# Kernel tuning notes

Measured on AMD Instinct MI355X. Metric: run time of the kernel, lower is better.

The kernel has to match this reference:

```python
import jax, jax.numpy as jnp
import numpy as np

DIM = 640
HEADS = 8
HEAD_DIM = 80
CROSS = 768
FF_INNER = 4 * DIM  # 2560
EPS = 1e-5
SCALE = HEAD_DIM ** -0.5


def _ln(x, w, b):
    m = jnp.mean(x, axis=-1, keepdims=True)
    v = jnp.var(x, axis=-1, keepdims=True)
    return (x - m) * jax.lax.rsqrt(v + EPS) * w + b


def _split_heads(x):  # [B,S,D] -> [B,H,S,dh]
    B, S, D = x.shape
    return x.reshape(B, S, HEADS, D // HEADS).transpose(0, 2, 1, 3)


def _merge_heads(x):  # [B,H,S,dh] -> [B,S,D]
    B, H, S, dh = x.shape
    return x.transpose(0, 2, 1, 3).reshape(B, S, H * dh)


def _mha(q, k, v):
    # q:[B,S,D] k,v:[B,Skv,D]
    qh, kh, vh = _split_heads(q), _split_heads(k), _split_heads(v)
    scores = jnp.einsum('bhqd,bhkd->bhqk', qh, kh) * SCALE
    probs = jax.nn.softmax(scores, axis=-1)
    out = jnp.einsum('bhqk,bhkd->bhqd', probs, vh)
    return _merge_heads(out)


def _forward(hidden_states, encoder_hidden_states, video_length, p):
    BF, S, D = hidden_states.shape
    f = video_length
    b = BF // f

    # ---- attn1: sparse causal self-attention ----
    x = _ln(hidden_states, p['ln1_w'], p['ln1_b'])
    q = x @ p['q1']
    k = x @ p['k1']
    v = x @ p['v1']
    former = jnp.concatenate([jnp.zeros((1,), jnp.int32), jnp.arange(f - 1, dtype=jnp.int32)])
    def gather_kv(t):  # [BF,S,D] -> [BF,2S,D]
        t = t.reshape(b, f, S, D)
        first = jnp.broadcast_to(t[:, 0:1], (b, f, S, D))
        prev = t[:, former]
        return jnp.concatenate([first, prev], axis=2).reshape(BF, 2 * S, D)
    k = gather_kv(k)
    v = gather_kv(v)
    attn1 = _mha(q, k, v) @ p['o1_w'] + p['o1_b']
    hidden_states = attn1 + hidden_states

    # ---- attn2: cross attention to text ----
    x = _ln(hidden_states, p['ln2_w'], p['ln2_b'])
    q = x @ p['q2']
    k = encoder_hidden_states @ p['k2']
    v = encoder_hidden_states @ p['v2']
    attn2 = _mha(q, k, v) @ p['o2_w'] + p['o2_b']
    hidden_states = attn2 + hidden_states

    # ---- feed-forward (geglu) ----
    x = _ln(hidden_states, p['ln3_w'], p['ln3_b'])
    proj = x @ p['ff_w1'] + p['ff_b1']
    h, gate = jnp.split(proj, 2, axis=-1)
    ff = (h * jax.nn.gelu(gate)) @ p['ff_w2'] + p['ff_b2']
    return ff + hidden_states


def setup_inputs() -> dict:
    key = jax.random.key(0)
    ks = jax.random.split(key, 20)
    s = lambda i, shape, scale=0.02: jax.random.normal(ks[i], shape, jnp.float32) * scale
    inp = {
        'hidden_states': jax.random.normal(ks[0], (8, 1024, DIM), jnp.float32),
        'encoder_hidden_states': jax.random.normal(ks[1], (8, 77, CROSS), jnp.float32),
        'video_length': 8,
        'ln1_w': jnp.ones((DIM,)), 'ln1_b': jnp.zeros((DIM,)),
        'q1': s(2, (DIM, DIM)), 'k1': s(3, (DIM, DIM)), 'v1': s(4, (DIM, DIM)),
        'o1_w': s(5, (DIM, DIM)), 'o1_b': jnp.zeros((DIM,)),
        'ln2_w': jnp.ones((DIM,)), 'ln2_b': jnp.zeros((DIM,)),
        'q2': s(6, (DIM, DIM)), 'k2': s(7, (CROSS, DIM)), 'v2': s(8, (CROSS, DIM)),
        'o2_w': s(9, (DIM, DIM)), 'o2_b': jnp.zeros((DIM,)),
        'ln3_w': jnp.ones((DIM,)), 'ln3_b': jnp.zeros((DIM,)),
        'ff_w1': s(10, (DIM, 2 * FF_INNER)), 'ff_b1': jnp.zeros((2 * FF_INNER,)),
        'ff_w2': s(11, (FF_INNER, DIM)), 'ff_b2': jnp.zeros((DIM,)),
    }
    return inp


def reference(hidden_states, encoder_hidden_states, video_length,
              ln1_w, ln1_b, q1, k1, v1, o1_w, o1_b,
              ln2_w, ln2_b, q2, k2, v2, o2_w, o2_b,
              ln3_w, ln3_b, ff_w1, ff_b1, ff_w2, ff_b2):
    p = dict(ln1_w=ln1_w, ln1_b=ln1_b, q1=q1, k1=k1, v1=v1, o1_w=o1_w, o1_b=o1_b,
             ln2_w=ln2_w, ln2_b=ln2_b, q2=q2, k2=k2, v2=v2, o2_w=o2_w, o2_b=o2_b,
             ln3_w=ln3_w, ln3_b=ln3_b, ff_w1=ff_w1, ff_b1=ff_b1, ff_w2=ff_w2, ff_b2=ff_b2)
    return _forward(hidden_states, encoder_hidden_states, video_length, p)
```

## Files before the change

### kernel.cpp

```cpp
#include <hip/hip_runtime.h>
#include <stdint.h>

#define TOK   8192
#define DIM   640
#define HEADS 8
#define HD    80
#define SEQ   1024
#define CROSS 768
#define ETOK  616
#define FFI   2560
#define SCALE 0.11180339887498949f

typedef unsigned short u16;
typedef unsigned int   u32;

using bf8   = __attribute__((ext_vector_type(8))) short;
using f32x4 = __attribute__((ext_vector_type(4))) float;

struct __align__(16) U4 { u32 x, y, z, w; };
struct __align__(8)  U2 { u32 x, y; };

__device__ __forceinline__ float bf2f(u16 u){
  union { u32 i; float f; } v; v.i = ((u32)u) << 16; return v.f;
}
__device__ __forceinline__ u16 f2bf(float f){
  union { float f; u32 i; } v; v.f = f;
  u32 r = v.i + 0x7fffu + ((v.i >> 16) & 1u);
  return (u16)(r >> 16);
}
__device__ __forceinline__ u32 cvtpk_bf16(float lo, float hi){
  u32 r; asm("v_cvt_pk_bf16_f32 %0, %1, %2" : "=v"(r) : "v"(lo), "v"(hi)); return r;
}
__device__ __forceinline__ float gelu_t(float x){
  float y = 0.7978845608028654f * (x + 0.044715f * x * x * x);
  float e = __expf(2.f * y);
  return 0.5f * x * (2.f - 2.f / (e + 1.f));
}

__device__ __forceinline__ void gl2lds16(const u16* g, u16* l){
  __builtin_amdgcn_global_load_lds(
      (const __attribute__((address_space(1))) void*)g,
      (__attribute__((address_space(3))) void*)l, 16, 0, 0);
}

__global__ void zero_k(u16* p){ p[threadIdx.x] = 0; }

struct CvtJob  { const float* s; u16* d; int n; };
struct CvtJobs { CvtJob j[11]; };
__global__ __launch_bounds__(256) void cvt_all(CvtJobs jobs)
{
  const CvtJob jb = jobs.j[blockIdx.y];
  for (long i = (long)blockIdx.x*256 + threadIdx.x; i < jb.n; i += (long)gridDim.x*256)
    jb.d[i] = f2bf(jb.s[i]);
}

struct TJob  { const float* s; u16* d; int R, C, srcLd, dstLd; };
struct TJobs { TJob j[10]; };
__global__ __launch_bounds__(256) void transpose_tiled(TJobs jobs)
{
  const TJob jb = jobs.j[blockIdx.y];
  const int tilesC = jb.C >> 6;
  const int nt = (jb.R >> 6) * tilesC;
  if ((int)blockIdx.x >= nt) return;
  const int tr = (blockIdx.x / tilesC) << 6, tc = (blockIdx.x % tilesC) << 6;
  __shared__ u16 t[64][65];
  const int tid = threadIdx.x;
  const int rr = tid >> 3, c8 = (tid & 7) * 8;
  #pragma unroll
  for (int p = 0; p < 2; ++p){
    const int r = rr + p*32;
    const float* s = &jb.s[(long)(tr + r)*jb.srcLd + tc + c8];
    #pragma unroll
    for (int j = 0; j < 8; ++j) t[r][c8 + j] = f2bf(s[j]);
  }
  __syncthreads();
  #pragma unroll
  for (int p = 0; p < 2; ++p){
    const int c = rr + p*32;
    u16 tmp[8];
    #pragma unroll
    for (int j = 0; j < 8; ++j) tmp[j] = t[c8 + j][c];
    *(U4*)&jb.d[(long)(tc + c)*jb.dstLd + tr + c8] = *(U4*)tmp;
  }
}

__global__ __launch_bounds__(256) void transpose_geglu(
    const float* __restrict__ src, u16* __restrict__ dst)
{
  __shared__ u16 t[64][65];
  const int ir0 = blockIdx.x << 6, k0 = blockIdx.y << 6;
  const int hc0 = ir0 >> 1;
  const int tid = threadIdx.x;
  const int rr = tid >> 3, c8 = (tid & 7) * 8;
  #pragma unroll
  for (int p = 0; p < 2; ++p){
    const int k = rr + p*32;
    const int scol = (c8 < 32) ? (hc0 + c8) : (FFI + hc0 + (c8 - 32));
    const float* s = &src[(long)(k0 + k)*(2*FFI) + scol];
    #pragma unroll
    for (int j = 0; j < 8; ++j){
      const int lc = c8 + j;
      const int grp = (lc < 32) ? 0 : 1;
      const int lg  = lc - grp*32;
      const int irl = (lg >> 4)*32 + grp*16 + (lg & 15);
      t[k][irl] = f2bf(s[j]);
    }
  }
  __syncthreads();
  #pragma unroll
  for (int p = 0; p < 2; ++p){
    const int c = rr + p*32;
    u16 tmp[8];
    #pragma unroll
    for (int j = 0; j < 8; ++j) tmp[j] = t[c8 + j][c];
    *(U4*)&dst[(long)(ir0 + c)*DIM + k0 + c8] = *(U4*)tmp;
  }
}

__global__ __launch_bounds__(256) void transpose_tile(
    const u16* __restrict__ src, u16* __restrict__ dst,
    int srcLd, int dstLd)
{
  __shared__ u16 t[64][65];
  const int tr = blockIdx.y << 6, tc = blockIdx.x << 6;
  const int tid = threadIdx.x;
  const int rr = tid >> 3, c8 = (tid & 7) * 8;
  #pragma unroll
  for (int p = 0; p < 2; ++p){
    const int r = rr + p*32;
    U4 v = *(const U4*)&src[(long)(tr + r)*srcLd + tc + c8];
    const u16* pv = (const u16*)&v;
    #pragma unroll
    for (int j = 0; j < 8; ++j) t[r][c8 + j] = pv[j];
  }
  __syncthreads();
  #pragma unroll
  for (int p = 0; p < 2; ++p){
    const int c = rr + p*32;
    u16 tmp[8];
    #pragma unroll
    for (int j = 0; j < 8; ++j) tmp[j] = t[c8 + j][c];
    *(U4*)&dst[(long)(tc + c)*dstLd + tr + c8] = *(U4*)tmp;
  }
}

__global__ __launch_bounds__(256) void transpose_v2(
    const u16* __restrict__ src, u16* __restrict__ dst)
{
  int idx = blockIdx.x*256 + threadIdx.x;
  if (idx >= DIM*640) return;
  int d = idx / 640, c = idx - d*640;
  int g = c / 80, j = c - g*80;
  u16 v = 0;
  if (j < 77) v = src[(long)(g*77 + j)*(2*DIM) + DIM + d];
  dst[(long)d*640 + c] = v;
}

__global__ __launch_bounds__(256) void ln_k(
    const void* __restrict__ src, const u16* __restrict__ w,
    const u16* __restrict__ b, u16* __restrict__ dst, int srcf32)
{
  const int wave = threadIdx.x >> 6, lane = threadIdx.x & 63;
  const long row = (long)blockIdx.x*4 + wave;
  float x[10];
  if (srcf32){
    const float* s = (const float*)src + row*DIM;
    #pragma unroll
    for (int j = 0; j < 5; ++j){
      float2 v = *(const float2*)&s[lane*2 + j*128];
      x[j*2] = v.x; x[j*2+1] = v.y;
    }
  } else {
    const u16* s = (const u16*)src + row*DIM;
    #pragma unroll
    for (int j = 0; j < 5; ++j){
      u32 v = *(const u32*)&s[lane*2 + j*128];
      x[j*2]   = bf2f((u16)(v & 0xffffu));
      x[j*2+1] = bf2f((u16)(v >> 16));
    }
  }
  float sum = 0.f;
  #pragma unroll
  for (int i = 0; i < 10; ++i) sum += x[i];
  #pragma unroll
  for (int d = 1; d < 64; d <<= 1) sum += __shfl_xor(sum, d, 64);
  const float mean = sum * (1.f/DIM);
  float vq = 0.f;
  #pragma unroll
  for (int i = 0; i < 10; ++i){ float dd = x[i] - mean; vq += dd*dd; }
  #pragma unroll
  for (int d = 1; d < 64; d <<= 1) vq += __shfl_xor(vq, d, 64);
  const float rs = rsqrtf(vq * (1.f/DIM) + 1e-5f);
  u16* q = dst + row*DIM;
  #pragma unroll
  for (int j = 0; j < 5; ++j){
    const int off = lane*2 + j*128;
    u32 wv = *(const u32*)&w[off];
    u32 bv = *(const u32*)&b[off];
    float o0 = (x[j*2]   - mean)*rs*bf2f((u16)(wv & 0xffffu)) + bf2f((u16)(bv & 0xffffu));
    float o1 = (x[j*2+1] - mean)*rs*bf2f((u16)(wv >> 16))     + bf2f((u16)(bv >> 16));
    *(u32*)&q[off] = (u32)f2bf(o0) | ((u32)f2bf(o1) << 16);
  }
}

template<int BN>
__global__ __launch_bounds__(256) void gemm_bt(
    const u16* __restrict__ A, const u16* __restrict__ BT, void* __restrict__ C,
    int M, int N, int K, int lda, int ldb, int ldc,
    const u16* __restrict__ bias, const void* __restrict__ res, int ldr,
    int resf32, int outf32)
{
  constexpr int NT  = BN/32;
  constexpr int BCH = BN/16;
  constexpr int BPW = BCH/4;
  constexpr int LPW = 2 + BPW;
  __shared__ __align__(16) u16 sA[3][8*512];
  __shared__ __align__(16) u16 sB[3][BCH*512];
  const int tid  = threadIdx.x;
  const int wave = tid >> 6, lane = tid & 63;
  const int quad = lane >> 4, l16 = lane & 15;
  const int m0 = blockIdx.y * 128, n0 = blockIdx.x * BN;
  const int wm = (wave >> 1) * 64, wn = (wave & 1) * (BN/2);
  const int srow = lane & 15;
  const int scol = (lane >> 4) * 8;

  long aoff[2];
  #pragma unroll
  for (int i = 0; i < 2; ++i){
    int r = m0 + (wave*2 + i)*16 + srow;
    r = r < M ? r : M - 1;
    aoff[i] = (long)r*lda + scol;
  }
  long boff[BPW];
  #pragma unroll
  for (int i = 0; i < BPW; ++i){
    int r = n0 + (wave*BPW + i)*16 + srow;
    boff[i] = (long)r*ldb + scol;
  }

  auto stage = [&](int ks, int buf){
    const int kk = ks*32;
    #pragma unroll
    for (int i = 0; i < 2; ++i)   gl2lds16(&A[aoff[i] + kk],  &sA[buf][(wave*2 + i)*512]);
    #pragma unroll
    for (int i = 0; i < BPW; ++i) gl2lds16(&BT[boff[i] + kk], &sB[buf][(wave*BPW + i)*512]);
  };

  const int NS = K >> 5;
  f32x4 acc[4][NT] = {};
  stage(0, 0);
  if (NS > 1) stage(1, 1);

  int cur = 0;
  for (int ks = 0; ks < NS; ++ks){
    if (ks < NS - 1) asm volatile("s_waitcnt vmcnt(%0)" :: "n"(LPW) : "memory");
    else             asm volatile("s_waitcnt vmcnt(0)" ::: "memory");
    __builtin_amdgcn_sched_barrier(0);
    __builtin_amdgcn_s_barrier();
    __builtin_amdgcn_sched_barrier(0);
    if (ks + 2 < NS){
      int nbuf = cur + 2; if (nbuf >= 3) nbuf -= 3;
      stage(ks + 2, nbuf);
    }
    bf8 a[4], b[NT];
    #pragma unroll
    for (int mt = 0; mt < 4; ++mt)  a[mt] = *(const bf8*)&sA[cur][((wm>>4) + mt)*512 + lane*8];
    #pragma unroll
    for (int nt = 0; nt < NT; ++nt) b[nt] = *(const bf8*)&sB[cur][((wn>>4) + nt)*512 + lane*8];
    #pragma unroll
    for (int mt = 0; mt < 4; ++mt)
      #pragma unroll
      for (int nt = 0; nt < NT; ++nt)
        acc[mt][nt] = __builtin_amdgcn_mfma_f32_16x16x32_bf16(a[mt], b[nt], acc[mt][nt], 0, 0, 0);
    cur = (cur == 2) ? 0 : cur + 1;
  }
  #pragma unroll
  for (int mt = 0; mt < 4; ++mt){
    const int rl = wm + mt*16 + quad*4;
    #pragma unroll
    for (int nt = 0; nt < NT; ++nt){
      const int col = n0 + wn + nt*16 + l16;
      float bv = bias ? bf2f(bias[col]) : 0.f;
      #pragma unroll
      for (int r = 0; r < 4; ++r){
        int row = m0 + rl + r;
        if (row < M){
          float v = acc[mt][nt][r] + bv;
          if (res) v += resf32 ? ((const float*)res)[(long)row*ldr + col]
                               : bf2f(((const u16*)res)[(long)row*ldr + col]);
          if (outf32) ((float*)C)[(long)row*ldc + col] = v;
          else        ((u16*)C) [(long)row*ldc + col] = f2bf(v);
        }
      }
    }
  }
}

__global__ __launch_bounds__(256) void gemm_geglu(
    const u16* __restrict__ A, const u16* __restrict__ W, u16* __restrict__ C,
    const u16* __restrict__ bias)
{
  __shared__ __align__(16) u16 sA[2][8*512];
  __shared__ __align__(16) u16 sB[2][8*512];
  const int tid  = threadIdx.x;
  const int wave = tid >> 6, lane = tid & 63;
  const int quad = lane >> 4, l16 = lane & 15;
  const int m0 = blockIdx.y * 128, n0 = blockIdx.x * 128;
  const int wm = (wave >> 1) * 64, wn = (wave & 1) * 64;
  const int srow = lane & 15;
  const int scol = (lane >> 4) * 8;

  long aoff[2], boff[2];
  #pragma unroll
  for (int i = 0; i < 2; ++i){
    aoff[i] = (long)(m0 + (wave*2 + i)*16 + srow)*DIM + scol;
    boff[i] = (long)(n0 + (wave*2 + i)*16 + srow)*DIM + scol;
  }

  f32x4 acc[4][4] = {};
  #pragma unroll
  for (int i = 0; i < 2; ++i){
    gl2lds16(&A[aoff[i]], &sA[0][(wave*2 + i)*512]);
    gl2lds16(&W[boff[i]], &sB[0][(wave*2 + i)*512]);
  }
  __syncthreads();

  int cur = 0;
  for (int k0 = 0; ; ){
    const int kn = k0 + 32;
    if (kn < DIM){
      #pragma unroll
      for (int i = 0; i < 2; ++i){
        gl2lds16(&A[aoff[i] + kn], &sA[cur^1][(wave*2 + i)*512]);
        gl2lds16(&W[boff[i] + kn], &sB[cur^1][(wave*2 + i)*512]);
      }
    }
    bf8 a[4], b[4];
    #pragma unroll
    for (int mt = 0; mt < 4; ++mt) a[mt] = *(const bf8*)&sA[cur][((wm>>4) + mt)*512 + lane*8];
    #pragma unroll
    for (int nt = 0; nt < 4; ++nt) b[nt] = *(const bf8*)&sB[cur][((wn>>4) + nt)*512 + lane*8];
    #pragma unroll
    for (int mt = 0; mt < 4; ++mt)
      #pragma unroll
      for (int nt = 0; nt < 4; ++nt)
        acc[mt][nt] = __builtin_amdgcn_mfma_f32_16x16x32_bf16(a[mt], b[nt], acc[mt][nt], 0, 0, 0);
    k0 = kn;
    if (k0 >= DIM) break;
    __syncthreads();
    cur ^= 1;
  }
  #pragma unroll
  for (int mt = 0; mt < 4; ++mt){
    const int rl = wm + mt*16 + quad*4;
    #pragma unroll
    for (int p = 0; p < 2; ++p){
      const int col = ((n0 + wn) >> 1) + p*16 + l16;
      const float bh = bf2f(bias[col]);
      const float bg = bf2f(bias[FFI + col]);
      #pragma unroll
      for (int r = 0; r < 4; ++r){
        int row = m0 + rl + r;
        float h = acc[mt][2*p][r]   + bh;
        float g = acc[mt][2*p+1][r] + bg;
        C[(long)row*FFI + col] = f2bf(h * gelu_t(g));
      }
    }
  }
}

template<int MODE>
__global__ __launch_bounds__(256) void attn_k(
    const u16* __restrict__ qbuf, const u16* __restrict__ kbuf,
    const u16* __restrict__ vT, u16* __restrict__ out,
    const u16* __restrict__ zblk)
{
  constexpr int QLD  = MODE ? DIM      : 3*DIM;
  constexpr int KLD  = MODE ? 2*DIM    : 3*DIM;
  constexpr int KCOL = MODE ? 0        : DIM;
  constexpr int VLD  = MODE ? DIM      : TOK;
  constexpr int NK   = MODE ? 77       : 2*SEQ;
  constexpr int NCH  = MODE ? 3        : 64;
  constexpr float C1   = SCALE * 1.4426950408889634f;
  constexpr float THRR = 8.0f / C1;

  const int qt = blockIdx.x, h = blockIdx.y, g = blockIdx.z;
  const int tid = threadIdx.x, wave = tid >> 6, lane = tid & 63;
  const int quad = lane >> 4, l16 = lane & 15;

  __shared__ __align__(16) u16 Kb[2][6*512];
  __shared__ __align__(16) u16 Vb[2][5*512];
  __shared__ __align__(16) u16 Ps[4][16*40];

  const int qrow0 = g*SEQ + qt*64;
  bf8 qf[3];
  {
    const long qbase = (long)(qrow0 + wave*16 + l16)*QLD + h*HD;
    #pragma unroll
    for (int ks = 0; ks < 3; ++ks){
      const int d = ks*32 + quad*8;
      const u16* src = (d < HD) ? &qbuf[qbase + d] : zblk;
      qf[ks] = *(const bf8*)src;
    }
  }

  const int former = (g == 0) ? 0 : (g - 1);

  const bool kc1v = (wave < 2);
  const int  vc0  = (wave + 2) & 3;
  const bool vc1v = (wave == 2);

  long ko[2] = {0,0}, koB[2] = {0,0}, vo[2] = {0,0}, voB[2] = {0,0};
  bool koob[2];
  #pragma unroll
  for (int j = 0; j < 2; ++j){
    const int ci = wave + 4*j;
    const int ck = ci/3, ks = ci - ck*3;
    const int d = ks*32 + quad*8;
    koob[j] = (d >= HD);
    if (MODE == 0){
      const int dcl = koob[j] ? 0 : d;
      const int row = ck*16 + l16;
      ko[j]  = (long)row*KLD + KCOL + h*HD + dcl;
      koB[j] = ko[j] + (long)former*SEQ*KLD;
    }
  }
  if (MODE == 0){
    vo[0]  = (long)(h*HD + vc0*16 + l16)*VLD + quad*8;
    vo[1]  = (long)(h*HD + 64    + l16)*VLD + quad*8;
    voB[0] = vo[0] + (long)former*SEQ;
    voB[1] = vo[1] + (long)former*SEQ;
  }

  auto stageM0 = [&](int buf){
    gl2lds16(koob[0] ? zblk : &kbuf[ko[0]], &Kb[buf][(wave)*512]);
    if (kc1v) gl2lds16(koob[1] ? zblk : &kbuf[ko[1]], &Kb[buf][(wave+4)*512]);
    gl2lds16(&vT[vo[0]], &Vb[buf][vc0*512]);
    if (vc1v) gl2lds16(&vT[vo[1]], &Vb[buf][4*512]);
    ko[0] += 32L*KLD; ko[1] += 32L*KLD;
    vo[0] += 32; vo[1] += 32;
  };
  auto stageM1 = [&](int c, int buf){
    #pragma unroll
    for (int ci = 0; ci < 6; ++ci){
      if ((ci & 3) == wave){
        const int ck = ci / 3, ks = ci % 3;
        const int d  = ks*32 + quad*8;
        const int rl = ck*16 + l16;
        int j = c*32 + rl; j = j < NK ? j : NK-1;
        const u16* src = (d < HD) ? &kbuf[((long)g*77 + j)*KLD + KCOL + h*HD + d] : zblk;
        gl2lds16(src, &Kb[buf][ci*512]);
      }
    }
    #pragma unroll
    for (int vi = 0; vi < 5; ++vi){
      if (((vi + 2) & 3) == wave){
        const int dd = vi*16 + l16;
        int key = c*32 + quad*8;
        const u16* src = (key < 80) ? &vT[(long)(h*HD + dd)*VLD + g*80 + key] : zblk;
        gl2lds16(src, &Vb[buf][vi*512]);
      }
    }
  };

  f32x4 o[5] = {};
  float mrun = -1e30f, lrun = 0.f, nmc = 0.f;

  if (MODE == 0) stageM0(0); else stageM1(0, 0);
  __syncthreads();
  int cur = 0;

  for (int c = 0; c < NCH; ++c){
    if (c + 1 < NCH){
      if (MODE == 0){
        if (c + 1 == 32){
          ko[0] = koB[0]; ko[1] = koB[1];
          vo[0] = voB[0]; vo[1] = voB[1];
        }
        stageM0(cur ^ 1);
      } else {
        stageM1(c + 1, cur ^ 1);
      }
    }

    f32x4 s0 = {}, s1 = {};
    #pragma unroll
    for (int ks = 0; ks < 3; ++ks){
      bf8 kf0 = *(const bf8*)&Kb[cur][ks*512     + lane*8];
      bf8 kf1 = *(const bf8*)&Kb[cur][(3+ks)*512 + lane*8];
      s0 = __builtin_amdgcn_mfma_f32_16x16x32_bf16(kf0, qf[ks], s0, 0, 0, 0);
      s1 = __builtin_amdgcn_mfma_f32_16x16x32_bf16(kf1, qf[ks], s1, 0, 0, 0);
    }

    if (MODE == 1){
      const int kg = c*32 + quad*4;
      #pragma unroll
      for (int r = 0; r < 4; ++r){
        if (kg + r >= NK)      s0[r] = -1e30f;
        if (kg + 16 + r >= NK) s1[r] = -1e30f;
      }
    }
    float mxs = fmaxf(fmaxf(fmaxf(s0[0],s0[1]), fmaxf(s0[2],s0[3])),
                      fmaxf(fmaxf(s1[0],s1[1]), fmaxf(s1[2],s1[3])));
    if (!__all(mxs - mrun <= THRR)){
      float mx = fmaxf(mxs, __shfl_xor(mxs, 16, 64));
      mx = fmaxf(mx, __shfl_xor(mx, 32, 64));
      float mn = fmaxf(mrun, mx);
      float al = exp2f((mrun - mn)*C1);
      mrun = mn; nmc = -mrun*C1;
      lrun *= al;
      float a0 = __shfl(al, quad*4 + 0, 16);
      float a1 = __shfl(al, quad*4 + 1, 16);
      float a2 = __shfl(al, quad*4 + 2, 16);
      float a3 = __shfl(al, quad*4 + 3, 16);
      #pragma unroll
      for (int dt = 0; dt < 5; ++dt){
        o[dt][0] *= a0; o[dt][1] *= a1; o[dt][2] *= a2; o[dt][3] *= a3;
      }
    }
    #pragma unroll
    for (int r = 0; r < 4; ++r){
      s0[r] = exp2f(__builtin_fmaf(s0[r], C1, nmc));
      s1[r] = exp2f(__builtin_fmaf(s1[r], C1, nmc));
    }
    lrun += ((s0[0]+s0[1])+(s0[2]+s0[3])) + ((s1[0]+s1[1])+(s1[2]+s1[3]));

    U2 w01, w23;
    w01.x = cvtpk_bf16(s0[0], s0[1]);  w01.y = cvtpk_bf16(s0[2], s0[3]);
    w23.x = cvtpk_bf16(s1[0], s1[1]);  w23.y = cvtpk_bf16(s1[2], s1[3]);
    U2* pr = (U2*)&Ps[wave][l16*40];
    pr[quad]     = w01;
    pr[4 + quad] = w23;
    asm volatile("s_waitcnt lgkmcnt(0)" ::: "memory");
    __builtin_amdgcn_sched_barrier(0);
    bf8 pf = *(const bf8*)&Ps[wave][l16*40 + quad*8];
    #pragma unroll
    for (int dt = 0; dt < 5; ++dt){
      bf8 vf = *(const bf8*)&Vb[cur][dt*512 + lane*8];
      o[dt] = __builtin_amdgcn_mfma_f32_16x16x32_bf16(pf, vf, o[dt], 0, 0, 0);
    }
    __syncthreads();
    cur ^= 1;
  }

  lrun += __shfl_xor(lrun, 16, 64);
  lrun += __shfl_xor(lrun, 32, 64);

  float linv[4];
  #pragma unroll
  for (int r = 0; r < 4; ++r)
    linv[r] = __builtin_amdgcn_rcpf(__shfl(lrun, quad*4 + r, 16));
  const int orow0 = qrow0 + wave*16 + quad*4;
  #pragma unroll
  for (int dt = 0; dt < 5; ++dt){
    const int col = h*HD + dt*16 + l16;
    #pragma unroll
    for (int r = 0; r < 4; ++r)
      out[(long)(orow0 + r)*DIM + col] = f2bf(o[dt][r] * linv[r]);
  }
}

extern "C" void kernel_launch(void* const* d_in, const int* in_sizes, int n_in,
                              void* d_out, int out_size, void* d_ws, size_t ws_size,
                              hipStream_t stream)
{
  const float* hidden = (const float*)d_in[0];
  const float* enc    = (const float*)d_in[1];
  const float* ln1w = (const float*)d_in[3],  *ln1b = (const float*)d_in[4];
  const float* q1   = (const float*)d_in[5],  *k1   = (const float*)d_in[6];
  const float* v1   = (const float*)d_in[7],  *o1w  = (const float*)d_in[8];
  const float* o1b  = (const float*)d_in[9];
  const float* ln2w = (const float*)d_in[10], *ln2b = (const float*)d_in[11];
  const float* q2   = (const float*)d_in[12], *k2   = (const float*)d_in[13];
  const float* v2   = (const float*)d_in[14], *o2w  = (const float*)d_in[15];
  const float* o2b  = (const float*)d_in[16];
  const float* ln3w = (const float*)d_in[17], *ln3b = (const float*)d_in[18];
  const float* fw1  = (const float*)d_in[19], *fb1  = (const float*)d_in[20];
  const float* fw2  = (const float*)d_in[21], *fb2  = (const float*)d_in[22];

  u16* ws = (u16*)d_ws;
  u16* Wqkv1T = ws;
  u16* o1T    = Wqkv1T + 1920*640;
  u16* q2T    = o1T    + 640*640;
  u16* Wkv2T  = q2T    + 640*640;
  u16* o2T    = Wkv2T  + 1280*768;
  u16* W1T    = o2T    + 640*640;
  u16* W2T    = W1T    + 5120*640;
  u16* xbuf   = W2T    + 640*2560;
  u16* qkv1   = xbuf   + (size_t)TOK*DIM;
  u16* v1T    = qkv1   + (size_t)TOK*3*DIM;
  u16* ffin   = qkv1;
  u16* attnb  = v1T    + (size_t)DIM*TOK;
  u16* hid2   = attnb  + (size_t)TOK*DIM;
  u16* hid3   = hid2   + (size_t)TOK*DIM;
  u16* q2buf  = hid3   + (size_t)TOK*DIM;
  u16* kv2    = q2buf  + (size_t)TOK*DIM;
  u16* v2T    = kv2    + (size_t)ETOK*2*DIM;
  u16* encm   = v2T    + 640*640 + 64;
  u16* bln1w  = encm   + (size_t)ETOK*CROSS;
  u16* bln1b  = bln1w + DIM;
  u16* bo1b   = bln1b + DIM;
  u16* bln2w  = bo1b  + DIM;
  u16* bln2b  = bln2w + DIM;
  u16* bo2b   = bln2b + DIM;
  u16* bln3w  = bo2b  + DIM;
  u16* bln3b  = bln3w + DIM;
  u16* bfb2   = bln3b + DIM;
  u16* bfb1   = bfb2  + DIM;
  u16* zblk   = bfb1  + 2*FFI;
  u16* wsend  = zblk  + 64;
  const size_t needed = ((size_t)(wsend - ws) + 64) * 2;
  if (ws_size < needed) return;

  dim3 blk(256);
  zero_k<<<1, 64, 0, stream>>>(zblk);

  CvtJobs jobs;
  jobs.j[0]  = { enc,  encm,  ETOK*CROSS };
  jobs.j[1]  = { ln1w, bln1w, DIM };
  jobs.j[2]  = { ln1b, bln1b, DIM };
  jobs.j[3]  = { o1b,  bo1b,  DIM };
  jobs.j[4]  = { ln2w, bln2w, DIM };
  jobs.j[5]  = { ln2b, bln2b, DIM };
  jobs.j[6]  = { o2b,  bo2b,  DIM };
  jobs.j[7]  = { ln3w, bln3w, DIM };
  jobs.j[8]  = { ln3b, bln3b, DIM };
  jobs.j[9]  = { fb2,  bfb2,  DIM };
  jobs.j[10] = { fb1,  bfb1,  2*FFI };
  cvt_all<<<dim3(64,11), blk, 0, stream>>>(jobs);

  TJobs tj;
  tj.j[0] = { q1,  Wqkv1T,            640, 640,  640,  640 };
  tj.j[1] = { k1,  Wqkv1T + 640*640,  640, 640,  640,  640 };
  tj.j[2] = { v1,  Wqkv1T + 1280*640, 640, 640,  640,  640 };
  tj.j[3] = { o1w, o1T,               640, 640,  640,  640 };
  tj.j[4] = { q2,  q2T,               640, 640,  640,  640 };
  tj.j[5] = { k2,  Wkv2T,             768, 640,  640,  768 };
  tj.j[6] = { v2,  Wkv2T + 640*768,   768, 640,  640,  768 };
  tj.j[7] = { o2w, o2T,               640, 640,  640,  640 };
  tj.j[8] = { fw2, W2T,               2560,640,  640,  2560 };
  tj.j[9] = { nullptr, nullptr, 0, 0, 0, 0 };
  transpose_tiled<<<dim3(400,9), blk, 0, stream>>>(tj);
  transpose_geglu<<<dim3(80,10), blk, 0, stream>>>(fw1, W1T);

  ln_k<<<TOK/4, blk, 0, stream>>>(hidden, bln1w, bln1b, xbuf, 1);
  gemm_bt<128><<<dim3(15,64), blk, 0, stream>>>(xbuf, Wqkv1T, qkv1,
      TOK, 3*DIM, DIM, DIM, DIM, 3*DIM, nullptr, nullptr, 0, 0, 0);
  transpose_tile<<<dim3(10,128), blk, 0, stream>>>(qkv1 + 2*DIM, v1T, 3*DIM, TOK);
  attn_k<0><<<dim3(16,8,8), blk, 0, stream>>>(qkv1, qkv1, v1T, attnb, zblk);
  gemm_bt<64><<<dim3(10,64), blk, 0, stream>>>(attnb, o1T, hid2,
      TOK, DIM, DIM, DIM, DIM, DIM, bo1b, hidden, DIM, 1, 0);

  ln_k<<<TOK/4, blk, 0, stream>>>(hid2, bln2w, bln2b, xbuf, 0);
  gemm_bt<64><<<dim3(10,64), blk, 0, stream>>>(xbuf, q2T, q2buf,
      TOK, DIM, DIM, DIM, DIM, DIM, nullptr, nullptr, 0, 0, 0);
  gemm_bt<64><<<dim3(20,5), blk, 0, stream>>>(encm, Wkv2T, kv2,
      ETOK, 2*DIM, CROSS, CROSS, CROSS, 2*DIM, nullptr, nullptr, 0, 0, 0);
  transpose_v2<<<dim3((DIM*640 + 255)/256), blk, 0, stream>>>(kv2, v2T);
  attn_k<1><<<dim3(16,8,8), blk, 0, stream>>>(q2buf, kv2, v2T, attnb, zblk);
  gemm_bt<64><<<dim3(10,64), blk, 0, stream>>>(attnb, o2T, hid3,
      TOK, DIM, DIM, DIM, DIM, DIM, bo2b, hid2, DIM, 0, 0);

  ln_k<<<TOK/4, blk, 0, stream>>>(hid3, bln3w, bln3b, xbuf, 0);
  gemm_geglu<<<dim3(40,64), blk, 0, stream>>>(xbuf, W1T, ffin, bfb1);
  gemm_bt<64><<<dim3(10,64), blk, 0, stream>>>(ffin, W2T, d_out,
      TOK, DIM, FFI, FFI, FFI, DIM, bfb2, hid3, DIM, 0, 1);
}
```

Baseline: 662.5 us.

## Triple-buffer GEGLU GEMM over multiple M tiles, tune attention exp and priority

The GEGLU GEMM now has each block walk four consecutive 128-row M tiles. It uses a three-stage LDS ring with explicit vmcnt waits and raw barriers, so loads stay in flight across tile boundaries, and the grid shrinks to match. In self-attention, frame 0 blocks stop after the first half of the keys, because its 'first' and 'previous' frames are the same frame and the duplicated keys do not change the softmax. Exponentials use raw v_exp_f32 instead of exp2f, and MFMA sections are wrapped in s_setprio to favour matrix issue. The risks are fewer GEGLU blocks, which lowers occupancy and parallelism, and the loss of exp2f range handling.

```diff
diff --git a/kernel.cpp b/kernel.cpp
--- a/kernel.cpp
+++ b/kernel.cpp
@@ -30,6 +30,9 @@
 }
 __device__ __forceinline__ u32 cvtpk_bf16(float lo, float hi){
   u32 r; asm("v_cvt_pk_bf16_f32 %0, %1, %2" : "=v"(r) : "v"(lo), "v"(hi)); return r;
+}
+__device__ __forceinline__ float exp2_hw(float x){
+  float r; asm("v_exp_f32 %0, %1" : "=v"(r) : "v"(x)); return r;
 }
 __device__ __forceinline__ float gelu_t(float x){
   float y = 0.7978845608028654f * (x + 0.044715f * x * x * x);
@@ -300,12 +303,16 @@
     const u16* __restrict__ A, const u16* __restrict__ W, u16* __restrict__ C,
     const u16* __restrict__ bias)
 {
-  __shared__ __align__(16) u16 sA[2][8*512];
-  __shared__ __align__(16) u16 sB[2][8*512];
+  constexpr int LPW = 4;
+  constexpr int NKS = DIM/32;
+  constexpr int MT  = 4;
+  __shared__ __align__(16) u16 sA[3][8*512];
+  __shared__ __align__(16) u16 sB[3][8*512];
   const int tid  = threadIdx.x;
   const int wave = tid >> 6, lane = tid & 63;
   const int quad = lane >> 4, l16 = lane & 15;
-  const int m0 = blockIdx.y * 128, n0 = blockIdx.x * 128;
+  const int n0 = blockIdx.x * 128;
+  const int mbase = blockIdx.y * (MT*128);
   const int wm = (wave >> 1) * 64, wn = (wave & 1) * 64;
   const int srow = lane & 15;
   const int scol = (lane >> 4) * 8;
@@ -313,59 +320,74 @@
   long aoff[2], boff[2];
   #pragma unroll
   for (int i = 0; i < 2; ++i){
-    aoff[i] = (long)(m0 + (wave*2 + i)*16 + srow)*DIM + scol;
+    aoff[i] = (long)(mbase + (wave*2 + i)*16 + srow)*DIM + scol;
     boff[i] = (long)(n0 + (wave*2 + i)*16 + srow)*DIM + scol;
   }
 
+  auto stage = [&](int t, int k, int buf){
+    const long adel = (long)t*(128*DIM) + k*32;
+    const long bdel = (long)k*32;
+    #pragma unroll
+    for (int i = 0; i < 2; ++i){
+      gl2lds16(&A[aoff[i] + adel], &sA[buf][(wave*2 + i)*512]);
+      gl2lds16(&W[boff[i] + bdel], &sB[buf][(wave*2 + i)*512]);
+    }
+  };
+
   f32x4 acc[4][4] = {};
-  #pragma unroll
-  for (int i = 0; i < 2; ++i){
-    gl2lds16(&A[aoff[i]], &sA[0][(wave*2 + i)*512]);
-    gl2lds16(&W[boff[i]], &sB[0][(wave*2 + i)*512]);
-  }
-  __syncthreads();
-
-  int cur = 0;
-  for (int k0 = 0; ; ){
-    const int kn = k0 + 32;
-    if (kn < DIM){
-      #pragma unroll
-      for (int i = 0; i < 2; ++i){
-        gl2lds16(&A[aoff[i] + kn], &sA[cur^1][(wave*2 + i)*512]);
-        gl2lds16(&W[boff[i] + kn], &sB[cur^1][(wave*2 + i)*512]);
-      }
-    }
-    bf8 a[4], b[4];
-    #pragma unroll
-    for (int mt = 0; mt < 4; ++mt) a[mt] = *(const bf8*)&sA[cur][((wm>>4) + mt)*512 + lane*8];
-    #pragma unroll
-    for (int nt = 0; nt < 4; ++nt) b[nt] = *(const bf8*)&sB[cur][((wn>>4) + nt)*512 + lane*8];
+  stage(0, 0, 0);
+  stage(0, 1, 1);
+
+  int cur = 0, nk = 2, ntile = 0;
+  for (int t = 0; t < MT; ++t){
+    for (int k = 0; k < NKS; ++k){
+      const bool last = (t == MT-1) && (k == NKS-1);
+      if (!last) asm volatile("s_waitcnt vmcnt(%0)" :: "n"(LPW) : "memory");
+      else       asm volatile("s_waitcnt vmcnt(0)" ::: "memory");
+      __builtin_amdgcn_sched_barrier(0);
+      __builtin_amdgcn_s_barrier();
+      __builtin_amdgcn_sched_barrier(0);
+      if (ntile < MT){
+        int nbuf = cur + 2; if (nbuf >= 3) nbuf -= 3;
+        stage(ntile, nk, nbuf);
+        if (++nk == NKS){ nk = 0; ++ntile; }
+      }
+      bf8 a[4], b[4];
+      #pragma unroll
+      for (int mt = 0; mt < 4; ++mt) a[mt] = *(const bf8*)&sA[cur][((wm>>4) + mt)*512 + lane*8];
+      #pragma unroll
+      for (int nt = 0; nt < 4; ++nt) b[nt] = *(const bf8*)&sB[cur][((wn>>4) + nt)*512 + lane*8];
+      #pragma unroll
+      for (int mt = 0; mt < 4; ++mt)
+        #pragma unroll
+        for (int nt = 0; nt < 4; ++nt)
+          acc[mt][nt] = __builtin_amdgcn_mfma_f32_16x16x32_bf16(a[mt], b[nt], acc[mt][nt], 0, 0, 0);
+      cur = (cur == 2) ? 0 : cur + 1;
+    }
+    const int m0 = mbase + t*128;
+    #pragma unroll
+    for (int mt = 0; mt < 4; ++mt){
+      const int rl = wm + mt*16 + quad*4;
+      #pragma unroll
+      for (int p = 0; p < 2; ++p){
+        const int col = ((n0 + wn) >> 1) + p*16 + l16;
+        const float bh = bf2f(bias[col]);
+        const float bg = bf2f(bias[FFI + col]);
+        #pragma unroll
+        for (int r = 0; r < 4; ++r){
+          int row = m0 + rl + r;
+          float h = acc[mt][2*p][r]   + bh;
+          float g = acc[mt][2*p+1][r] + bg;
+          C[(long)row*FFI + col] = f2bf(h * gelu_t(g));
+        }
+      }
+    }
     #pragma unroll
     for (int mt = 0; mt < 4; ++mt)
       #pragma unroll
       for (int nt = 0; nt < 4; ++nt)
-        acc[mt][nt] = __builtin_amdgcn_mfma_f32_16x16x32_bf16(a[mt], b[nt], acc[mt][nt], 0, 0, 0);
-    k0 = kn;
-    if (k0 >= DIM) break;
-    __syncthreads();
-    cur ^= 1;
-  }
-  #pragma unroll
-  for (int mt = 0; mt < 4; ++mt){
-    const int rl = wm + mt*16 + quad*4;
-    #pragma unroll
-    for (int p = 0; p < 2; ++p){
-      const int col = ((n0 + wn) >> 1) + p*16 + l16;
-      const float bh = bf2f(bias[col]);
-      const float bg = bf2f(bias[FFI + col]);
-      #pragma unroll
-      for (int r = 0; r < 4; ++r){
-        int row = m0 + rl + r;
-        float h = acc[mt][2*p][r]   + bh;
-        float g = acc[mt][2*p+1][r] + bg;
-        C[(long)row*FFI + col] = f2bf(h * gelu_t(g));
-      }
-    }
+        #pragma unroll
+        for (int r = 0; r < 4; ++r) acc[mt][nt][r] = 0.f;
   }
 }
 
@@ -387,6 +409,7 @@
   const int qt = blockIdx.x, h = blockIdx.y, g = blockIdx.z;
   const int tid = threadIdx.x, wave = tid >> 6, lane = tid & 63;
   const int quad = lane >> 4, l16 = lane & 15;
+  const int NCHeff = (MODE == 0 && g == 0) ? 32 : NCH;
 
   __shared__ __align__(16) u16 Kb[2][6*512];
   __shared__ __align__(16) u16 Vb[2][5*512];
@@ -470,8 +493,8 @@
   __syncthreads();
   int cur = 0;
 
-  for (int c = 0; c < NCH; ++c){
-    if (c + 1 < NCH){
+  for (int c = 0; c < NCHeff; ++c){
+    if (c + 1 < NCHeff){
       if (MODE == 0){
         if (c + 1 == 32){
           ko[0] = koB[0]; ko[1] = koB[1];
@@ -484,6 +507,7 @@
     }
 
     f32x4 s0 = {}, s1 = {};
+    __builtin_amdgcn_s_setprio(1);
     #pragma unroll
     for (int ks = 0; ks < 3; ++ks){
       bf8 kf0 = *(const bf8*)&Kb[cur][ks*512     + lane*8];
@@ -491,6 +515,7 @@
       s0 = __builtin_amdgcn_mfma_f32_16x16x32_bf16(kf0, qf[ks], s0, 0, 0, 0);
       s1 = __builtin_amdgcn_mfma_f32_16x16x32_bf16(kf1, qf[ks], s1, 0, 0, 0);
     }
+    __builtin_amdgcn_s_setprio(0);
 
     if (MODE == 1){
       const int kg = c*32 + quad*4;
@@ -506,7 +531,7 @@
       float mx = fmaxf(mxs, __shfl_xor(mxs, 16, 64));
       mx = fmaxf(mx, __shfl_xor(mx, 32, 64));
       float mn = fmaxf(mrun, mx);
-      float al = exp2f((mrun - mn)*C1);
+      float al = exp2_hw((mrun - mn)*C1);
       mrun = mn; nmc = -mrun*C1;
       lrun *= al;
       float a0 = __shfl(al, quad*4 + 0, 16);
@@ -520,8 +545,8 @@
     }
     #pragma unroll
     for (int r = 0; r < 4; ++r){
-      s0[r] = exp2f(__builtin_fmaf(s0[r], C1, nmc));
-      s1[r] = exp2f(__builtin_fmaf(s1[r], C1, nmc));
+      s0[r] = exp2_hw(__builtin_fmaf(s0[r], C1, nmc));
+      s1[r] = exp2_hw(__builtin_fmaf(s1[r], C1, nmc));
     }
     lrun += ((s0[0]+s0[1])+(s0[2]+s0[3])) + ((s1[0]+s1[1])+(s1[2]+s1[3]));
 
@@ -534,11 +559,13 @@
     asm volatile("s_waitcnt lgkmcnt(0)" ::: "memory");
     __builtin_amdgcn_sched_barrier(0);
     bf8 pf = *(const bf8*)&Ps[wave][l16*40 + quad*8];
+    __builtin_amdgcn_s_setprio(1);
     #pragma unroll
     for (int dt = 0; dt < 5; ++dt){
       bf8 vf = *(const bf8*)&Vb[cur][dt*512 + lane*8];
       o[dt] = __builtin_amdgcn_mfma_f32_16x16x32_bf16(pf, vf, o[dt], 0, 0, 0);
     }
+    __builtin_amdgcn_s_setprio(0);
     __syncthreads();
     cur ^= 1;
   }
@@ -662,7 +689,7 @@
       TOK, DIM, DIM, DIM, DIM, DIM, bo2b, hid2, DIM, 0, 0);
 
   ln_k<<<TOK/4, blk, 0, stream>>>(hid3, bln3w, bln3b, xbuf, 0);
-  gemm_geglu<<<dim3(40,64), blk, 0, stream>>>(xbuf, W1T, ffin, bfb1);
+  gemm_geglu<<<dim3(40,16), blk, 0, stream>>>(xbuf, W1T, ffin, bfb1);
   gemm_bt<64><<<dim3(10,64), blk, 0, stream>>>(ffin, W2T, d_out,
       TOK, DIM, FFI, FFI, FFI, DIM, bfb2, hid3, DIM, 0, 1);
 }
```

New measurement: 703.2 us. 1.06x slower.
